# Kernel tuning notes

Measured on AMD Instinct MI355X. Metric: run time of the kernel, lower is better.

## Reference

```python
import jax, jax.numpy as jnp
import numpy as np

B, N, DE, H, DH = 2, 1024, 1024, 16, 64
DK = H * DH  # total complex qkv dim per stream
MIN_EXP = -30.0
EPS = 1e-4


def setup_inputs():
    key = jax.random.key(0)
    ks = jax.random.split(key, 8)

    def g(i, shape, sc=1.0):
        return jax.random.normal(ks[i], shape, jnp.float32) * sc

    # RoPE-style per-head frequencies for the conjugate-paired half-dims
    freqs = 10000.0 ** (-np.arange(DH // 2, dtype=np.float64) / (DH // 2))
    omega = jnp.asarray(np.tile(freqs[None, :], (H, 1)), jnp.float32)
    return {
        "x": g(0, (B, N, DE)),
        "Wq": g(1, (DE, 2 * DK), 1.0 / np.sqrt(DE)),
        "Wk": g(2, (DE, 2 * DK), 1.0 / np.sqrt(DE)),
        "Wv": g(3, (DE, 2 * DK), 1.0 / np.sqrt(DE)),
        "Wo": g(4, (2 * DK, DE), 1.0 / np.sqrt(2 * DK)),
        "omega": omega,
        "mu_raw": g(5, (H,)) - 2.0,          # pre-sigmoid decay rates
        "sigma_raw": g(6, (H,)),              # pre-softplus process noise
        "eta_raw": jnp.ones((H,), jnp.float32),
        "gamma_raw": jnp.ones((H,), jnp.float32),
        "tau": jnp.ones((H,), jnp.float32),   # inverse temperature
        "nu_raw": jnp.ones((H,), jnp.float32) * 4.0,  # robustness dof
    }


def reference(x, Wq, Wk, Wv, Wo, omega, mu_raw, sigma_raw, eta_raw, gamma_raw, tau, nu_raw):
    B_, N_, _ = x.shape
    H_, d_half = omega.shape
    DH_ = 2 * d_half
    DKt = H_ * DH_

    def cproj(W):
        z = x @ W                          # [B,N,2D] real/imag packed
        D = W.shape[1] // 2
        zc = jax.lax.complex(z[..., :D], z[..., D:])
        return zc.reshape(B_, N_, H_, DH_)

    q, k, v = cproj(Wq), cproj(Wk), cproj(Wv)

    # complex-conjugate-constrained rotations: omega stacked as [w, -w]
    om = jnp.concatenate([omega, -omega], axis=-1)              # [H,DH]
    t = jnp.arange(N_, dtype=jnp.float32)
    ang = t[:, None, None] * om[None]                           # [N,H,DH]
    phase = jax.lax.complex(jnp.cos(ang), jnp.sin(ang))
    qr = q * phase[None]
    kr = k * phase[None]

    # isotropic SDE decay kernel  E_rel = exp(-mu * |t_i - t_j|)
    mu = jax.nn.sigmoid(mu_raw) + EPS                           # [H]
    dt = jnp.abs(t[:, None] - t[None, :])                       # [N,N]
    E = jnp.exp(jnp.clip(-mu[:, None, None] * dt[None], MIN_EXP, 0.0))  # [H,N,N]

    # Re<q_i, Phi(dt) k_j>  (rotation carried by phases, decay by E)
    s = jnp.einsum('bihd,bjhd->bhij', qr, jnp.conj(kr)).real    # [B,H,N,N]
    qn = (q.real ** 2 + q.imag ** 2).sum(-1).transpose(0, 2, 1)  # [B,H,N]
    kn = (k.real ** 2 + k.imag ** 2).sum(-1).transpose(0, 2, 1)

    # Lyapunov-propagated uncertainty: P(dt) = sigma^2/(2mu)(1 - E^2) + eta^2 + gamma^2
    sigma_sq = jax.nn.softplus(sigma_raw)
    eta_sq = jax.nn.softplus(eta_raw)
    gamma_sq = jax.nn.softplus(gamma_raw)
    V = (sigma_sq / (2.0 * mu))[:, None, None] * (1.0 - E * E) \
        + (eta_sq + gamma_sq)[:, None, None]                    # [H,N,N]

    # per-head Mahalanobis residual under the SDE forecast
    maha = jnp.maximum(qn[..., None] + (E * E)[None] * kn[:, :, None, :]
                       - 2.0 * E[None] * s, 0.0) / V[None]      # [B,H,N,N]

    # robust nu-thresholding (Student-t style) + Gaussian normalization term
    nu = jax.nn.softplus(nu_raw)
    coef = (-0.5 * tau * (nu + DH_))[None, :, None, None]
    logits = coef * jnp.log1p(maha / nu[None, :, None, None]) \
             - 0.5 * DH_ * jnp.log(V)[None]

    causal = (t[:, None] >= t[None, :])
    logits = jnp.where(causal[None, None], logits, -jnp.inf)
    A = jax.nn.softmax(logits, axis=-1)                         # [B,H,N,N]

    out = jnp.einsum('bhij,bjhd->bihd', A.astype(v.dtype), v)   # complex [B,N,H,DH]
    y = jnp.concatenate([out.real.reshape(B_, N_, DKt),
                         out.imag.reshape(B_, N_, DKt)], axis=-1)
    return y @ Wo                                               # [B,N,DE]
```

## Files before the change

### kernel.cpp

```cpp
#include <hip/hip_runtime.h>
#include <math.h>

#define BB      2
#define NN      1024
#define DE_     1024
#define HH      16
#define TWO_DK  2048
#define PK      4194304
#define TBLR    1092

typedef float f32x4  __attribute__((ext_vector_type(4)));
typedef short bf16x8 __attribute__((ext_vector_type(8)));

__device__ __forceinline__ short f2bf(float f) {
    unsigned u = __float_as_uint(f);
    unsigned r = (u + 0x7fffu + ((u >> 16) & 1u)) >> 16;
    return (short)r;
}

__device__ __forceinline__ float fexp2(float x) { return __builtin_amdgcn_exp2f(x); }
__device__ __forceinline__ float flog2(float x) { return __builtin_amdgcn_logf(x); }

#define GLDS16(g, l) __builtin_amdgcn_global_load_lds(                        \
    (const __attribute__((address_space(1))) unsigned int*)(g),               \
    (__attribute__((address_space(3))) unsigned int*)(l), 16, 0, 0)
#define GLDS4(g, l) __builtin_amdgcn_global_load_lds(                         \
    (const __attribute__((address_space(1))) unsigned int*)(g),               \
    (__attribute__((address_space(3))) unsigned int*)(l), 4, 0, 0)

__global__ __launch_bounds__(256) void prep(
    const float* __restrict__ x,
    const float* __restrict__ Wq, const float* __restrict__ Wk,
    const float* __restrict__ Wv, const float* __restrict__ Wo,
    const float* __restrict__ mu_raw, const float* __restrict__ sigma_raw,
    const float* __restrict__ eta_raw, const float* __restrict__ gamma_raw,
    short* __restrict__ xb, short* __restrict__ wt, short* __restrict__ wot,
    float4* __restrict__ tbl) {
    const int z = blockIdx.z;
    if (z == 4) {
        const int flat = blockIdx.y * 32 + blockIdx.x;
        const int i = (flat * 256 + threadIdx.x) * 8;
        float4 v0 = *(const float4*)&x[i];
        float4 v1 = *(const float4*)&x[i + 4];
        short4 o0, o1;
        o0.x = f2bf(v0.x); o0.y = f2bf(v0.y); o0.z = f2bf(v0.z); o0.w = f2bf(v0.w);
        o1.x = f2bf(v1.x); o1.y = f2bf(v1.y); o1.z = f2bf(v1.z); o1.w = f2bf(v1.w);
        *(short4*)&xb[i] = o0; *(short4*)&xb[i + 4] = o1;
        return;
    }
    if (z == 3 && blockIdx.x >= 16) {
        const int idx = blockIdx.y * 16 + (blockIdx.x - 16);
        if (idx >= 80) return;
        const int h = idx / 5, rb = idx % 5;
        const int r = rb * 256 + threadIdx.x;
        if (r >= TBLR) return;
        const float mu = 1.f / (1.f + expf(-mu_raw[h])) + 1e-4f;
        const float Ac = log1pf(expf(sigma_raw[h])) / (2.f * mu);
        const float Cc = log1pf(expf(eta_raw[h])) + log1pf(expf(gamma_raw[h]));
        const float arg = fminf(fmaxf(-mu * (float)(r - 64), -30.f), 0.f);
        const float E   = expf(arg);
        const float V   = fmaf(Ac, 1.f - E * E, Cc);
        tbl[h * TBLR + r] = make_float4(2.f * E, 1.f / V, -32.f * log2f(V), E * E);
        return;
    }
    const float* in; short* out; int R, C;
    if (z < 3) { if (blockIdx.y >= 16) return;
                 in = (z == 0) ? Wq : (z == 1) ? Wk : Wv;
                 out = wt + (size_t)z * 2097152; R = 1024; C = 2048; }
    else       { in = Wo; out = wot; R = 2048; C = 1024; }
    __shared__ float t[64][65];
    const int c0 = blockIdx.x * 64, r0 = blockIdx.y * 64;
    const int tr = threadIdx.x >> 4, tc4 = (threadIdx.x & 15) * 4;
#pragma unroll
    for (int s = 0; s < 4; ++s) {
        const int r = tr + s * 16;
        float4 v = *(const float4*)&in[(size_t)(r0 + r) * C + c0 + tc4];
        t[r][tc4] = v.x; t[r][tc4 + 1] = v.y; t[r][tc4 + 2] = v.z; t[r][tc4 + 3] = v.w;
    }
    __syncthreads();
#pragma unroll
    for (int s = 0; s < 4; ++s) {
        const int oc = tr + s * 16;
        short4 o;
        o.x = f2bf(t[tc4 + 0][oc]); o.y = f2bf(t[tc4 + 1][oc]);
        o.z = f2bf(t[tc4 + 2][oc]); o.w = f2bf(t[tc4 + 3][oc]);
        *(short4*)&out[(size_t)(c0 + oc) * R + r0 + tc4] = o;
    }
}

__global__ __launch_bounds__(256) void gemm_qkv_rot2(
    const short* __restrict__ A, const short* __restrict__ wt,
    const float* __restrict__ omega,
    short* __restrict__ qb, short* __restrict__ kb, short* __restrict__ vtb,
    float* __restrict__ qn_, float* __restrict__ kn_) {
    __shared__ __align__(16) short As[128 * 64];
    __shared__ __align__(16) short Bs[128 * 64];
    __shared__ float sN[2][128];
    const int tid = threadIdx.x;
    const int m0  = blockIdx.x * 128;
    const int h   = blockIdx.y;
    const short* W = wt + (size_t)blockIdx.z * 2097152;

    const short* aP[4]; const short* bP[4]; int ldsoff[4];
#pragma unroll
    for (int i = 0; i < 4; ++i) {
        const int c   = i * 256 + tid;
        const int row = c >> 3;
        const int src = ((c & 7) ^ (row & 7)) << 3;
        ldsoff[i] = c * 8;
        aP[i] = A + (size_t)(m0 + row) * 1024 + src;
        const int t_ = row >> 5, u_ = (row >> 4) & 1, dcol = t_ * 16 + (row & 15);
        bP[i] = W + (size_t)(u_ * 1024 + h * 64 + dcol) * 1024 + src;
    }

    const int lane = tid & 63, w = tid >> 6;
    const int wr = (w >> 1) * 64, hsel = w & 1, wc = hsel * 64;
    const int fr = lane & 15;
    const int fo = (lane >> 4) << 3;
    const int sw = (fr & 7) << 3;

    f32x4 acc[4][4];
#pragma unroll
    for (int a = 0; a < 4; ++a)
#pragma unroll
        for (int b = 0; b < 4; ++b) acc[a][b] = (f32x4){0.f, 0.f, 0.f, 0.f};

    for (int k0 = 0; k0 < 1024; k0 += 64) {
#pragma unroll
        for (int i = 0; i < 4; ++i) GLDS16(aP[i] + k0, &As[ldsoff[i]]);
#pragma unroll
        for (int i = 0; i < 4; ++i) GLDS16(bP[i] + k0, &Bs[ldsoff[i]]);
        __syncthreads();
#pragma unroll
        for (int ks = 0; ks < 64; ks += 32) {
            bf16x8 af[4], bf[4];
#pragma unroll
            for (int a = 0; a < 4; ++a)
                af[a] = *(const bf16x8*)&As[(wr + a * 16 + fr) * 64 + ((ks + fo) ^ sw)];
#pragma unroll
            for (int b = 0; b < 4; ++b)
                bf[b] = *(const bf16x8*)&Bs[(wc + b * 16 + fr) * 64 + ((ks + fo) ^ sw)];
#pragma unroll
            for (int a = 0; a < 4; ++a)
#pragma unroll
                for (int b = 0; b < 4; ++b)
                    acc[a][b] = __builtin_amdgcn_mfma_f32_16x16x32_bf16(
                        af[a], bf[b], acc[a][b], 0, 0, 0);
        }
        __syncthreads();
    }

    const int cq = (lane >> 4) * 4, l15 = lane & 15;
    const int bh  = (m0 >> 10) * 16 + h;
    const int nb0 = (m0 & 1023) + wr + cq;

    if (blockIdx.z == 2) {
#pragma unroll
        for (int a = 0; a < 4; ++a) {
#pragma unroll
            for (int b = 0; b < 4; ++b) {
                const int cl = wc + b * 16;
                const int dd = ((cl >> 4) & 1) * 64 + (cl >> 5) * 16 + l15;
                short4 o;
                o.x = f2bf(acc[a][b][0]); o.y = f2bf(acc[a][b][1]);
                o.z = f2bf(acc[a][b][2]); o.w = f2bf(acc[a][b][3]);
                *(short4*)&vtb[((size_t)bh * 128 + dd) * 1024 + nb0 + a * 16] = o;
            }
        }
        return;
    }
    float* nout = (blockIdx.z == 0) ? qn_ : kn_;
    short* obuf = (blockIdx.z == 0) ? qb  : kb;

#pragma unroll
    for (int a = 0; a < 4; ++a) {
        float ns[4] = {0.f, 0.f, 0.f, 0.f};
#pragma unroll
        for (int b = 0; b < 4; ++b)
#pragma unroll
            for (int r = 0; r < 4; ++r)
                ns[r] = fmaf(acc[a][b][r], acc[a][b][r], ns[r]);
#pragma unroll
        for (int m2 = 1; m2 < 16; m2 <<= 1)
#pragma unroll
            for (int r = 0; r < 4; ++r) ns[r] += __shfl_xor(ns[r], m2);
        if (l15 == 0)
#pragma unroll
            for (int r = 0; r < 4; ++r) sN[hsel][wr + a * 16 + cq + r] = ns[r];
    }
    __syncthreads();
    if (tid < 128)
        nout[(size_t)bh * 1024 + (m0 & 1023) + tid] = sN[0][tid] + sN[1][tid];

#pragma unroll
    for (int p = 0; p < 2; ++p) {
        const int d = (hsel * 2 + p) * 16 + l15;
        const float om = (d < 32) ? omega[h * 32 + d] : -omega[h * 32 + d - 32];
#pragma unroll
        for (int a = 0; a < 4; ++a) {
#pragma unroll
            for (int r = 0; r < 4; ++r) {
                const int n2 = nb0 + a * 16 + r;
                float sn, cs;
                __sincosf((float)n2 * om, &sn, &cs);
                const float re = acc[a][2 * p][r], im = acc[a][2 * p + 1][r];
                short* orow = obuf + ((size_t)bh * 1024 + n2) * 128;
                orow[d]      = f2bf(re * cs - im * sn);
                orow[64 + d] = f2bf(re * sn + im * cs);
            }
        }
    }
}

__global__ __launch_bounds__(256) void attn_mfma(
    const short* __restrict__ qr, const short* __restrict__ kr,
    const short* __restrict__ vt,
    const float* __restrict__ qn, const float* __restrict__ kn,
    const float4* __restrict__ tbl,
    const float* __restrict__ tau_p, const float* __restrict__ nu_raw,
    short* __restrict__ y) {
    __shared__ __align__(16) short Ks[2][64 * 128];
    __shared__ __align__(16) short Vs[2][128 * 64];
    __shared__ __align__(16) short Ps[64 * 72];
    __shared__ __align__(16) float4 sT[2][128];
    __shared__ float sKn[2][64];

    const int bx  = blockIdx.x;
    const int xcd = bx & 7;
    const int j   = bx >> 3;
    const int b2  = j & 3;
    const int itr = j >> 2;
    const int bh  = xcd * 4 + (b2 & 1) * 2 + (itr >> 3);
    const int h   = bh & 15;
    const int it  = ((itr & 7) << 1) | (b2 >> 1);
    const int i0  = it * 64;

    const int tid  = threadIdx.x;
    const int lane = tid & 63, w = tid >> 6;
    const int quad = lane >> 4, l15 = lane & 15;

    const float nu     = log1pf(expf(nu_raw[h]));
    const float coef   = -0.5f * tau_p[h] * (nu + 64.0f);
    const float inv_nu = 1.f / nu;

    const short* Qb  = qr + (size_t)bh * NN * 128;
    const short* Kb  = kr + (size_t)bh * NN * 128;
    const short* Vtb = vt + (size_t)bh * 128 * NN;

#define STAGE(JT, P) do {                                                     \
        const int j0_ = (JT) * 64, dt0_ = i0 - j0_;                           \
        _Pragma("unroll")                                                     \
        for (int i_ = 0; i_ < 4; ++i_) {                                      \
            const int c_ = i_ * 256 + tid, row_ = c_ >> 4;                    \
            const int src_ = ((c_ & 15) ^ (row_ & 7)) * 8;                    \
            GLDS16(Kb + (size_t)(j0_ + row_) * 128 + src_, &Ks[P][c_ * 8]);   \
        }                                                                     \
        _Pragma("unroll")                                                     \
        for (int i_ = 0; i_ < 4; ++i_) {                                      \
            const int c_ = i_ * 256 + tid, d_ = c_ >> 3;                      \
            const int src_ = ((c_ & 7) ^ (d_ & 7)) * 8;                       \
            GLDS16(Vtb + (size_t)d_ * NN + j0_ + src_, &Vs[P][c_ * 8]);       \
        }                                                                     \
        if (w == 0) {                                                         \
            GLDS16(tbl + h * TBLR + 1 + dt0_ + lane, &sT[P][lane]);           \
            GLDS16(tbl + h * TBLR + 65 + dt0_ + lane, &sT[P][64 + lane]);     \
        } else if (w == 1) {                                                  \
            GLDS4(kn + (size_t)bh * NN + j0_ + lane, &sKn[P][lane]);          \
        }                                                                     \
    } while (0)

    bf16x8 qf[4];
    const int arow = i0 + w * 16 + l15;
#pragma unroll
    for (int ks = 0; ks < 4; ++ks)
        qf[ks] = *(const bf16x8*)&Qb[(size_t)arow * 128 + ks * 32 + quad * 8];

    float mrow[4];
    f32x4 o[8];
    f32x4 o9 = (f32x4){0.f, 0.f, 0.f, 0.f};
#pragma unroll
    for (int r = 0; r < 4; ++r) mrow[r] = -INFINITY;
#pragma unroll
    for (int s = 0; s < 8; ++s) o[s] = (f32x4){0.f, 0.f, 0.f, 0.f};
    float qn4[4];
#pragma unroll
    for (int r = 0; r < 4; ++r)
        qn4[r] = qn[(size_t)bh * NN + i0 + w * 16 + quad * 4 + r];

    const bf16x8 onesv = (bf16x8){0x3F80, 0x3F80, 0x3F80, 0x3F80,
                                  0x3F80, 0x3F80, 0x3F80, 0x3F80};

    STAGE(0, 0);
    __syncthreads();

    for (int jt = 0; jt <= it; ++jt) {
        const int p = jt & 1;
        if (jt < it) STAGE(jt + 1, 1 - p);

        f32x4 sAcc[4];
#pragma unroll
        for (int s = 0; s < 4; ++s) sAcc[s] = (f32x4){0.f, 0.f, 0.f, 0.f};
#pragma unroll
        for (int ks = 0; ks < 4; ++ks) {
#pragma unroll
            for (int s = 0; s < 4; ++s) {
                const int brow = s * 16 + l15;
                bf16x8 bK = *(const bf16x8*)&Ks[p][brow * 128 +
                                                  (((ks * 4 + quad) ^ (brow & 7)) * 8)];
                sAcc[s] = __builtin_amdgcn_mfma_f32_16x16x32_bf16(qf[ks], bK, sAcc[s], 0, 0, 0);
            }
        }

        float al[4];
        bool anyr = false;
#pragma unroll
        for (int r = 0; r < 4; ++r) {
            const int row = w * 16 + quad * 4 + r;
            float lg[4];
#pragma unroll
            for (int s = 0; s < 4; ++s) {
                const int col = s * 16 + l15;
                const float4 T = sT[p][row - col + 63];
                const float sv = sAcc[s][r];
                const float t1 = fmaf(T.w, sKn[p][col], qn4[r]);
                const float maha = fmaxf(fmaf(-T.x, sv, t1), 0.f) * T.y;
                float v = fmaf(coef, flog2(fmaf(maha, inv_nu, 1.f)), T.z);
                if (jt == it && col > row) v = -INFINITY;
                lg[s] = v;
            }
            float mx = fmaxf(fmaxf(lg[0], lg[1]), fmaxf(lg[2], lg[3]));
            mx = fmaxf(mx, __shfl_xor(mx, 1));
            mx = fmaxf(mx, __shfl_xor(mx, 2));
            mx = fmaxf(mx, __shfl_xor(mx, 4));
            mx = fmaxf(mx, __shfl_xor(mx, 8));
            const bool resc = mx > mrow[r] + 16.f;
            const float mu_ = resc ? mx : mrow[r];
            al[r] = resc ? fexp2(mrow[r] - mx) : 1.f;
            mrow[r] = mu_;
            anyr = anyr || resc;
#pragma unroll
            for (int s = 0; s < 4; ++s) {
                const float pv = fexp2(lg[s] - mu_);
                Ps[row * 72 + s * 16 + l15] = f2bf(pv);
            }
        }
        if (anyr) {
#pragma unroll
            for (int s = 0; s < 8; ++s)
#pragma unroll
                for (int r = 0; r < 4; ++r) o[s][r] *= al[r];
#pragma unroll
            for (int r = 0; r < 4; ++r) o9[r] *= al[r];
        }

#pragma unroll
        for (int jc = 0; jc < 2; ++jc) {
            bf16x8 aP = *(const bf16x8*)&Ps[(w * 16 + l15) * 72 + jc * 32 + quad * 8];
#pragma unroll
            for (int sub = 0; sub < 8; ++sub) {
                const int d = sub * 16 + l15;
                bf16x8 bV = *(const bf16x8*)&Vs[p][d * 64 + (((jc * 4 + quad) ^ (d & 7)) * 8)];
                o[sub] = __builtin_amdgcn_mfma_f32_16x16x32_bf16(aP, bV, o[sub], 0, 0, 0);
            }
            o9 = __builtin_amdgcn_mfma_f32_16x16x32_bf16(aP, onesv, o9, 0, 0, 0);
        }
        if (jt < it) __syncthreads();
    }
#undef STAGE

#pragma unroll
    for (int r = 0; r < 4; ++r) {
        const float inv = 1.f / o9[r];
        const size_t base = ((size_t)bh * NN + i0 + w * 16 + quad * 4 + r) * 128;
#pragma unroll
        for (int sub = 0; sub < 8; ++sub)
            y[base + sub * 16 + l15] = f2bf(o[sub][r] * inv);
    }
}

__global__ __launch_bounds__(256) void gemm_out64(
    const short* __restrict__ yb, const short* __restrict__ wot,
    float* __restrict__ out) {
    __shared__ __align__(16) short As[64 * 64];
    __shared__ __align__(16) short Bs[64 * 64];
    const int tid = threadIdx.x;
    const int m0  = blockIdx.x * 64;
    const int n0  = blockIdx.y * 64;
    const int bb  = m0 >> 10;

    int aPre[2], aOff[2]; const short* bP[2];
#pragma unroll
    for (int i = 0; i < 2; ++i) {
        const int c = i * 256 + tid, row = c >> 3;
        const int src = ((c & 7) ^ (row & 7)) << 3;
        aPre[i] = ((m0 & 1023) + row) * 128 + src;
        bP[i] = wot + (size_t)(n0 + row) * 2048 + src;
        aOff[i] = c * 8;
    }

    const int lane = tid & 63, w = tid >> 6;
    const int wr = (w >> 1) * 32, wc = (w & 1) * 32;
    const int fr = lane & 15;
    const int fo = (lane >> 4) << 3;
    const int sw = (fr & 7) << 3;

    f32x4 acc[2][2];
#pragma unroll
    for (int a = 0; a < 2; ++a)
#pragma unroll
        for (int b = 0; b < 2; ++b) acc[a][b] = (f32x4){0.f, 0.f, 0.f, 0.f};

    for (int k0 = 0; k0 < 2048; k0 += 64) {
        const int hh = (k0 >> 6) & 15, im = k0 >> 10;
        const short* ab = yb + ((size_t)(bb * 16 + hh) << 17) + im * 64;
#pragma unroll
        for (int i = 0; i < 2; ++i) GLDS16(ab + aPre[i], &As[aOff[i]]);
#pragma unroll
        for (int i = 0; i < 2; ++i) GLDS16(bP[i] + k0, &Bs[aOff[i]]);
        __syncthreads();
#pragma unroll
        for (int ks = 0; ks < 64; ks += 32) {
            bf16x8 af[2], bf[2];
#pragma unroll
            for (int a = 0; a < 2; ++a)
                af[a] = *(const bf16x8*)&As[(wr + a * 16 + fr) * 64 + ((ks + fo) ^ sw)];
#pragma unroll
            for (int b = 0; b < 2; ++b)
                bf[b] = *(const bf16x8*)&Bs[(wc + b * 16 + fr) * 64 + ((ks + fo) ^ sw)];
#pragma unroll
            for (int a = 0; a < 2; ++a)
#pragma unroll
                for (int b = 0; b < 2; ++b)
                    acc[a][b] = __builtin_amdgcn_mfma_f32_16x16x32_bf16(
                        af[a], bf[b], acc[a][b], 0, 0, 0);
        }
        __syncthreads();
    }

    const int cq = (lane >> 4) * 4, l15 = lane & 15;
#pragma unroll
    for (int a = 0; a < 2; ++a)
#pragma unroll
        for (int b = 0; b < 2; ++b)
#pragma unroll
            for (int r = 0; r < 4; ++r)
                out[(size_t)(m0 + wr + a * 16 + cq + r) * 1024 +
                    (n0 + wc + b * 16 + l15)] = acc[a][b][r];
}

extern "C" void kernel_launch(void* const* d_in, const int* in_sizes, int n_in,
                              void* d_out, int out_size, void* d_ws, size_t ws_size,
                              hipStream_t stream) {
    const float* x         = (const float*)d_in[0];
    const float* Wq        = (const float*)d_in[1];
    const float* Wk        = (const float*)d_in[2];
    const float* Wv        = (const float*)d_in[3];
    const float* Wo        = (const float*)d_in[4];
    const float* omega     = (const float*)d_in[5];
    const float* mu_raw    = (const float*)d_in[6];
    const float* sigma_raw = (const float*)d_in[7];
    const float* eta_raw   = (const float*)d_in[8];
    const float* gamma_raw = (const float*)d_in[9];
    const float* tau       = (const float*)d_in[10];
    const float* nu_raw    = (const float*)d_in[11];
    float* out = (float*)d_out;

    short*  qb  = (short*)d_ws;
    short*  kb  = qb + PK;
    short*  vtb = kb + PK;
    float*  qn  = (float*)(vtb + PK);
    float*  kn  = qn + 32768;
    float4* tbl = (float4*)(kn + 32768);
    short*  wot = (short*)(tbl + HH * TBLR);
    short*  wt  = wot + 2097152;
    short*  xb  = wt + 3 * 2097152;
    short*  yb  = wt;

    prep<<<dim3(32, 32, 5), 256, 0, stream>>>(
        x, Wq, Wk, Wv, Wo, mu_raw, sigma_raw, eta_raw, gamma_raw,
        xb, wt, wot, tbl);
    gemm_qkv_rot2<<<dim3(16, 16, 3), 256, 0, stream>>>(
        xb, wt, omega, qb, kb, vtb, qn, kn);
    attn_mfma<<<dim3(512), 256, 0, stream>>>(
        qb, kb, vtb, qn, kn, tbl, tau, nu_raw, yb);
    gemm_out64<<<dim3(32, 16), 256, 0, stream>>>(yb, wot, out);
}
```

Before: 210.9 us.

## Split long causal attention rows into two KV chunks and merge partials

The attention kernel now launches 768 blocks. Query tiles 8-15 have their key range split into two chunks via constant tables that pair and balance work, so each block processes a similar number of key tiles. Partial outputs and log-sum-exp values go to scratch, and a new merge kernel combines them with softmax rescaling. This targets tail imbalance in causal attention, at the cost of an extra launch, scratch traffic and an extra bf16 rounding of the partial outputs.

After: 201.4 us. -4.5%, faster.

```diff
diff --git a/kernel.cpp b/kernel.cpp
--- a/kernel.cpp
+++ b/kernel.cpp
@@ -17,6 +17,9 @@
     unsigned r = (u + 0x7fffu + ((u >> 16) & 1u)) >> 16;
     return (short)r;
 }
+__device__ __forceinline__ float bf2f(short v) {
+    return __uint_as_float(((unsigned)(unsigned short)v) << 16);
+}
 
 __device__ __forceinline__ float fexp2(float x) { return __builtin_amdgcn_exp2f(x); }
 __device__ __forceinline__ float flog2(float x) { return __builtin_amdgcn_logf(x); }
@@ -27,6 +30,15 @@
 #define GLDS4(g, l) __builtin_amdgcn_global_load_lds(                         \
     (const __attribute__((address_space(1))) unsigned int*)(g),               \
     (__attribute__((address_space(3))) unsigned int*)(l), 4, 0, 0)
+
+__constant__ int jIT[24] = {7,14,15,15, 6,12,13,13,14, 5,10,11,11,12,
+                            4, 8, 9, 9,10, 3, 8, 2, 1, 0};
+__constant__ int jJ0[24] = {0, 0, 0, 8, 0, 0, 0, 7, 8, 0, 0, 0, 6, 7,
+                            0, 0, 0, 5, 6, 0, 5, 0, 0, 0};
+__constant__ int jJ1[24] = {7, 7, 7,15, 6, 6, 6,13,14, 5, 5, 5,11,12,
+                            4, 4, 4, 9,10, 3, 8, 2, 1, 0};
+__constant__ int jPS[24] = {0, 1, 1, 2, 0, 1, 1, 2, 2, 0, 1, 1, 2, 2,
+                            0, 1, 1, 2, 2, 0, 2, 0, 0, 0};
 
 __global__ __launch_bounds__(256) void prep(
     const float* __restrict__ x,
@@ -218,22 +230,25 @@
     const float* __restrict__ qn, const float* __restrict__ kn,
     const float4* __restrict__ tbl,
     const float* __restrict__ tau_p, const float* __restrict__ nu_raw,
-    short* __restrict__ y) {
+    short* __restrict__ y, short* __restrict__ po0, float* __restrict__ pml) {
     __shared__ __align__(16) short Ks[2][64 * 128];
     __shared__ __align__(16) short Vs[2][128 * 64];
     __shared__ __align__(16) short Ps[64 * 72];
     __shared__ __align__(16) float4 sT[2][128];
     __shared__ float sKn[2][64];
 
-    const int bx  = blockIdx.x;
-    const int xcd = bx & 7;
-    const int j   = bx >> 3;
-    const int b2  = j & 3;
-    const int itr = j >> 2;
-    const int bh  = xcd * 4 + (b2 & 1) * 2 + (itr >> 3);
-    const int h   = bh & 15;
-    const int it  = ((itr & 7) << 1) | (b2 >> 1);
-    const int i0  = it * 64;
+    const int bx   = blockIdx.x;
+    const int xcd  = bx & 7;
+    const int rest = bx >> 3;
+    const int jrk  = rest >> 2;
+    const int bh   = xcd * 4 + (rest & 3);
+    const int h    = bh & 15;
+    const int it   = jIT[jrk];
+    const int j0j  = jJ0[jrk];
+    const int j1j  = jJ1[jrk];
+    const int psel = jPS[jrk];
+    const int i0   = it * 64;
+    const int pq   = bh * 8 + (it - 8);
 
     const int tid  = threadIdx.x;
     const int lane = tid & 63, w = tid >> 6;
@@ -290,12 +305,12 @@
     const bf16x8 onesv = (bf16x8){0x3F80, 0x3F80, 0x3F80, 0x3F80,
                                   0x3F80, 0x3F80, 0x3F80, 0x3F80};
 
-    STAGE(0, 0);
+    STAGE(j0j, 0);
     __syncthreads();
 
-    for (int jt = 0; jt <= it; ++jt) {
-        const int p = jt & 1;
-        if (jt < it) STAGE(jt + 1, 1 - p);
+    for (int jt = j0j; jt <= j1j; ++jt) {
+        const int p = (jt - j0j) & 1;
+        if (jt < j1j) STAGE(jt + 1, 1 - p);
 
         f32x4 sAcc[4];
 #pragma unroll
@@ -364,17 +379,49 @@
             }
             o9 = __builtin_amdgcn_mfma_f32_16x16x32_bf16(aP, onesv, o9, 0, 0, 0);
         }
-        if (jt < it) __syncthreads();
+        if (jt < j1j) __syncthreads();
     }
 #undef STAGE
 
+    short* dst = (psel == 1) ? po0 : y;
+    const size_t rbase = (psel == 1) ? (size_t)pq * 64 : ((size_t)bh * NN + i0);
 #pragma unroll
     for (int r = 0; r < 4; ++r) {
+        const int lrow = w * 16 + quad * 4 + r;
         const float inv = 1.f / o9[r];
-        const size_t base = ((size_t)bh * NN + i0 + w * 16 + quad * 4 + r) * 128;
+        const size_t base = (rbase + lrow) * 128;
 #pragma unroll
         for (int sub = 0; sub < 8; ++sub)
-            y[base + sub * 16 + l15] = f2bf(o[sub][r] * inv);
+            dst[base + sub * 16 + l15] = f2bf(o[sub][r] * inv);
+        if (psel != 0 && l15 == 0)
+            pml[(pq * 2 + (psel - 1)) * 64 + lrow] = mrow[r] + flog2(o9[r]);
+    }
+}
+
+__global__ __launch_bounds__(256) void attn_merge(
+    const short* __restrict__ po0, const float* __restrict__ pml,
+    short* __restrict__ y) {
+    const int qs = blockIdx.x;
+    const int bh = qs >> 3, it = (qs & 7) + 8;
+    const int t = threadIdx.x;
+    const int row = t >> 2, dc = (t & 3) * 32;
+    const float m1 = pml[(qs * 2 + 0) * 64 + row];
+    const float m2 = pml[(qs * 2 + 1) * 64 + row];
+    const float mx = fmaxf(m1, m2);
+    const float w1 = fexp2(m1 - mx), w2 = fexp2(m2 - mx);
+    const float inv = 1.f / (w1 + w2);
+    const float a = w1 * inv, b = w2 * inv;
+    const short* s1 = po0 + ((size_t)qs * 64 + row) * 128 + dc;
+    short*       s2 = y + ((size_t)bh * NN + it * 64 + row) * 128 + dc;
+#pragma unroll
+    for (int i = 0; i < 32; i += 8) {
+        bf16x8 v1 = *(const bf16x8*)(s1 + i);
+        bf16x8 v2 = *(const bf16x8*)(s2 + i);
+        bf16x8 ov;
+#pragma unroll
+        for (int k = 0; k < 8; ++k)
+            ov[k] = f2bf(a * bf2f(v1[k]) + b * bf2f(v2[k]));
+        *(bf16x8*)(s2 + i) = ov;
     }
 }
 
@@ -475,13 +522,16 @@
     short*  wt  = wot + 2097152;
     short*  xb  = wt + 3 * 2097152;
     short*  yb  = wt;
+    short*  po0 = wt + 4194304;
+    float*  pml = (float*)xb;
 
     prep<<<dim3(32, 32, 5), 256, 0, stream>>>(
         x, Wq, Wk, Wv, Wo, mu_raw, sigma_raw, eta_raw, gamma_raw,
         xb, wt, wot, tbl);
     gemm_qkv_rot2<<<dim3(16, 16, 3), 256, 0, stream>>>(
         xb, wt, omega, qb, kb, vtb, qn, kn);
-    attn_mfma<<<dim3(512), 256, 0, stream>>>(
-        qb, kb, vtb, qn, kn, tbl, tau, nu_raw, yb);
+    attn_mfma<<<dim3(768), 256, 0, stream>>>(
+        qb, kb, vtb, qn, kn, tbl, tau, nu_raw, yb, po0, pml);
+    attn_merge<<<dim3(256), 256, 0, stream>>>(po0, pml, yb);
     gemm_out64<<<dim3(32, 16), 256, 0, stream>>>(yb, wot, out);
 }
```
